# Optimization experiments

Hardware: AMD Instinct MI355X
Metric: run time of the kernel (lower is better)

The kernel has to match this reference:

```python
import jax, jax.numpy as jnp
import numpy as np

FM = 64      # feature_maps
QM = 64      # query_maps
ROUNDS = 16  # test_rounds (training=False path)
NV = 50000   # n_vars
NC = 210000  # n_clauses
NE = 630000  # literal-clause edges (3-SAT)
NG = 32      # batched graphs
EPS = 1e-6


def _leaky(x):
    return jax.nn.leaky_relu(x, negative_slope=0.2)


def _mlp2(x, W0, b0, W1, b1):
    return _leaky(x @ W0 + b0) @ W1 + b1


def _mlp3(x, W0, b0, W1, b1, W2, b2):
    return _leaky(_leaky(x @ W0 + b0) @ W1 + b1) @ W2 + b2


def _pair_norm(x, seg, n_seg):
    # PairNorm with per-graph mean subtraction and per-graph variance scaling
    cnt = jax.ops.segment_sum(jnp.ones((x.shape[0], 1), x.dtype), seg, num_segments=n_seg)
    mean = jax.ops.segment_sum(x, seg, num_segments=n_seg) / cnt
    xc = x - mean[seg]
    var = jax.ops.segment_sum(xc * xc, seg, num_segments=n_seg) / cnt
    return xc * jax.lax.rsqrt(var + EPS)[seg]


def _glorot(k, shape):
    return (jax.random.normal(k, shape) * np.sqrt(2.0 / (shape[0] + shape[1]))).astype(jnp.float32)


def setup_inputs() -> dict:
    key = jax.random.key(0)
    ks = jax.random.split(key, 16)
    lit_idx = jax.random.randint(ks[0], (NE,), 0, 2 * NV)
    clause_idx = jnp.repeat(jnp.arange(NC), NE // NC)  # 3 literals per clause
    var_gid = jnp.sort(jax.random.randint(ks[1], (NV,), 0, NG))
    clause_gid = jnp.sort(jax.random.randint(ks[2], (NC,), 0, NG))
    noise = jax.random.normal(ks[3], (ROUNDS, NV, 4), dtype=jnp.float32)
    inp = dict(lit_idx=lit_idx, clause_idx=clause_idx, var_gid=var_gid,
               clause_gid=clause_gid, noise=noise)
    # variables_query: MLP(2, QM, QM), input FM+4
    inp['qW0'] = _glorot(ks[4], (FM + 4, QM)); inp['qb0'] = jnp.zeros((QM,), jnp.float32)
    inp['qW1'] = _glorot(ks[5], (QM, QM));     inp['qb1'] = jnp.zeros((QM,), jnp.float32)
    # clause_mlp: MLP(2, 2*FM, FM+QM), input FM+QM
    inp['cW0'] = _glorot(ks[6], (FM + QM, 2 * FM));   inp['cb0'] = jnp.zeros((2 * FM,), jnp.float32)
    inp['cW1'] = _glorot(ks[7], (2 * FM, FM + QM));   inp['cb1'] = jnp.zeros((FM + QM,), jnp.float32)
    # update_gate: MLP(3, 2*FM, FM), input QM+FM+QM+QM
    inp['uW0'] = _glorot(ks[8], (FM + 3 * QM, 2 * FM)); inp['ub0'] = jnp.zeros((2 * FM,), jnp.float32)
    inp['uW1'] = _glorot(ks[9], (2 * FM, 2 * FM));      inp['ub1'] = jnp.zeros((2 * FM,), jnp.float32)
    inp['uW2'] = _glorot(ks[10], (2 * FM, FM));         inp['ub2'] = jnp.zeros((FM,), jnp.float32)
    # clauses_output: MLP(2, FM, 1)
    inp['oW0'] = _glorot(ks[11], (FM, FM)); inp['ob0'] = jnp.zeros((FM,), jnp.float32)
    inp['oW1'] = _glorot(ks[12], (FM, 1));  inp['ob1'] = jnp.zeros((1,), jnp.float32)
    return inp


def reference(lit_idx, clause_idx, var_gid, clause_gid, noise,
              qW0, qb0, qW1, qb1, cW0, cb0, cW1, cb1,
              uW0, ub0, uW1, ub1, uW2, ub2, oW0, ob0, oW1, ob1):
    # literal degrees: sparse row-sums of adj_matrix
    lit_degree = jax.ops.segment_sum(jnp.ones((NE,), jnp.float32), lit_idx,
                                     num_segments=2 * NV)[:, None]  # [2V,1]
    degree_weight = jax.lax.rsqrt(jnp.maximum(lit_degree, 1.0))
    var_degree_weight = 4.0 * jax.lax.rsqrt(jnp.maximum(lit_degree[:NV] + lit_degree[NV:], 1.0))

    def clause_loss_fn(query):
        # unsat_cnf_clauses_loss: clause value = exp(-sum softplus(lit))
        lits = jax.nn.softplus(jnp.concatenate([query, -query], axis=0))  # [2V,QM]
        cv = jax.ops.segment_sum(lits[lit_idx], clause_idx, num_segments=NC)
        return jnp.exp(-cv)  # [C,QM]

    def step_loss_fn(query):
        cl = clause_loss_fn(query)
        return jnp.sum(cl), cl

    def body(carry, noise_t):
        variables, clauses = carry
        v1 = jnp.concatenate([variables, noise_t], axis=-1)          # [V, FM+4]
        query = _mlp2(v1, qW0, qb0, qW1, qb1)                        # [V, QM]
        (_, clauses_loss), vgrad = jax.value_and_grad(step_loss_fn, has_aux=True)(query)
        vgrad = vgrad * var_degree_weight
        clauses_loss = clauses_loss * 4.0
        clause_unit = jnp.concatenate([clauses, clauses_loss], axis=-1)  # [C, FM+QM]
        clause_data = _mlp2(clause_unit, cW0, cb0, cW1, cb1)             # [C, FM+QM]
        variables_loss_all = clause_data[:, :QM]
        new_clause = _pair_norm(clause_data[:, QM:], clause_gid, NG) * 0.25
        clauses = new_clause + 0.1 * clauses
        # variables_loss = adj_matrix @ variables_loss_all  (gather per edge, scatter to literals)
        variables_loss = jax.ops.segment_sum(variables_loss_all[clause_idx], lit_idx,
                                             num_segments=2 * NV) * degree_weight
        unit = jnp.concatenate([vgrad, variables, variables_loss[:NV], variables_loss[NV:]], axis=-1)
        new_vars = _pair_norm(_mlp3(unit, uW0, ub0, uW1, ub1, uW2, ub2), var_gid, NG) * 0.25
        variables = new_vars + 0.1 * variables
        logits = _mlp2(clauses, oW0, ob0, oW1, ob1)  # [C,1]
        variables = jax.lax.stop_gradient(variables) * 0.2 + variables * 0.8
        clauses = jax.lax.stop_gradient(clauses) * 0.2 + clauses * 0.8
        return (variables, clauses), logits

    init = (jnp.ones((NV, FM), jnp.float32), jnp.ones((NC, FM), jnp.float32))
    _, step_logits = jax.lax.scan(body, init, noise)
    last_logits = step_logits[-1]  # inference path: last round's logits [C,1]
    return (jnp.squeeze(jax.nn.sigmoid(last_logits), axis=-1),
            jnp.squeeze(jax.nn.softplus(last_logits), axis=-1))
```

## Files before the change

### kernel.cpp

```cpp
#include <hip/hip_runtime.h>
#include <math.h>

typedef unsigned short u16;
typedef unsigned int u32;
typedef _Float16 f16;
typedef f16 f16x8 __attribute__((ext_vector_type(8)));
typedef f16 f16x4 __attribute__((ext_vector_type(4)));
typedef float f32x4 __attribute__((ext_vector_type(4)));

constexpr int kNV = 50000;
constexpr int kNC = 210000;
constexpr int kNE = 630000;
constexpr int kNG = 32;
constexpr int kRounds = 16;
constexpr float kEps = 1e-6f;

constexpr int kCmlpB = (kNC + 63)/64;
constexpr int kVmlpB = (kNV + 63)/64;
constexpr int kUpdCB = kNC*64/1024;

__device__ __forceinline__ float bf2f(u16 v){ return __uint_as_float(((u32)v)<<16); }
__device__ __forceinline__ u16 f2bf(float f){
  u32 x = __float_as_uint(f);
  x += 0x7FFFu + ((x>>16)&1u);
  return (u16)(x>>16);
}
__device__ __forceinline__ u16 f2h(float v){
  union { f16 h; u16 u; } cv; cv.h = (f16)v; return cv.u;
}
__device__ __forceinline__ float h2f(u16 v){
  union { u16 u; f16 h; } cv; cv.u = v; return (float)cv.h;
}
__device__ __forceinline__ float leaky(float x){ return x>0.f ? x : 0.2f*x; }
__device__ __forceinline__ float softplusf(float x){
  return fmaxf(x,0.f) + __logf(1.f + __expf(-fabsf(x)));
}

struct Buf { void* p; int f32; };
__device__ __forceinline__ float ldb(Buf b, size_t i){
  return b.f32 ? ((const float*)b.p)[i] : bf2f(((const u16*)b.p)[i]);
}
__device__ __forceinline__ void stb(Buf b, size_t i, float v){
  if (b.f32) ((float*)b.p)[i] = v; else ((u16*)b.p)[i] = f2bf(v);
}
__device__ __forceinline__ float4 ldb4(Buf b, size_t i){
  if (b.f32) return *(const float4*)((const float*)b.p + i);
  u32 a = *(const u32*)((const u16*)b.p + i);
  u32 c = *(const u32*)((const u16*)b.p + i + 2);
  float4 r; r.x=bf2f((u16)a); r.y=bf2f((u16)(a>>16)); r.z=bf2f((u16)c); r.w=bf2f((u16)(c>>16));
  return r;
}
__device__ __forceinline__ void stb4(Buf b, size_t i, float4 v){
  if (b.f32){ *(float4*)((float*)b.p + i) = v; return; }
  u32 a = (u32)f2bf(v.x) | ((u32)f2bf(v.y)<<16);
  u32 c = (u32)f2bf(v.z) | ((u32)f2bf(v.w)<<16);
  *(u32*)((u16*)b.p + i) = a; *(u32*)((u16*)b.p + i + 2) = c;
}

constexpr int WP_C0 = 0;
constexpr int WP_C1 = 16384;
constexpr int WP_U0 = 32768;
constexpr int WP_U1 = 65536;
constexpr int WP_U2 = 81920;
constexpr int WP_Q0 = 90112;
constexpr int WP_Q1 = 96256;
constexpr int WP_TOT= 100352;

#define XS_STR 136

__global__ __launch_bounds__(256) void k_init(Buf vars, Buf cls, int* cnt, int* cur,
                                              double* stats, int* vst, int* ven,
                                              int* cst, int* cen){
  int i = blockIdx.x*256 + threadIdx.x;
  if (i < kNV*64) stb(vars, i, 1.f);
  stb(cls, i, 1.f);
  if (i < 2*kNV){ cnt[i]=0; cur[i]=0; }
  if (i < 16384) stats[i]=0.0;
  if (i < kNG){ vst[i]=0; ven[i]=0; cst[i]=0; cen[i]=0; }
}

__global__ __launch_bounds__(256) void k_wprep(
  const float* __restrict__ cW0, const float* __restrict__ cW1,
  const float* __restrict__ uW0, const float* __restrict__ uW1,
  const float* __restrict__ uW2,
  const float* __restrict__ qW0, const float* __restrict__ qW1,
  u16* __restrict__ wp){
  int i = blockIdx.x*256 + threadIdx.x;
  if (i < 16384){ int n=i>>7, k=i&127; wp[i] = f2h(cW0[k*128+n]); }
  else if (i < 32768){ int j=i-16384; int n=j>>7, k=j&127; wp[i] = f2h(cW1[k*128+n]); }
  else if (i < 65536){ int j=i-32768; int n=j>>8, k=j&255; wp[i] = f2h(uW0[k*128+n]); }
  else if (i < 81920){ int j=i-65536; int n=j>>7, k=j&127; wp[i] = f2h(uW1[k*128+n]); }
  else if (i < 90112){ int j=i-81920; int n=j>>7, k=j&127; wp[i] = f2h(uW2[k*64+n]); }
  else if (i < 96256){ int j=i-90112; int n=j/96, k=j%96; wp[i] = (k<68)? f2h(qW0[k*64+n]) : (u16)0; }
  else if (i < WP_TOT){ int j=i-96256; int n=j>>6, k=j&63; wp[i] = f2h(qW1[k*64+n]); }
}

__global__ __launch_bounds__(256) void k_hist(const int* __restrict__ lit,
                                              const int* __restrict__ vgid,
// ... 43 lines not shown
  if (i < 2*kNV){
    rs[i] += bsum[blockIdx.x];
    int c = cnt[i]; if (c<1) c=1;
    dw[i] = rsqrtf((float)c);
  }
  if (i < kNV){
    int c = cnt[i] + cnt[i+kNV]; if (c<1) c=1;
    vdw[i] = 4.f*rsqrtf((float)c);
  }
}

__global__ __launch_bounds__(256) void k_fill(const int* __restrict__ lit,
                                              const int* __restrict__ cidx,
                                              const int* __restrict__ rs, int* cur, int* csr){
  int e = blockIdx.x*256 + threadIdx.x;
  if (e < kNE){
    int l = lit[e];
    int p = atomicAdd(&cur[l], 1);
    csr[rs[l]+p] = cidx[e];
  }
}

__global__ __launch_bounds__(256) void k_query(
  Buf vars, const float* __restrict__ noise_r,
  const u16* __restrict__ Q0T, const u16* __restrict__ Q1T,
  f16* __restrict__ SP,
  Buf nvb, const int* __restrict__ vgid,
  const int* __restrict__ vst, const int* __restrict__ ven,
  const double* __restrict__ vSo, const double* __restrict__ vQo,
  double* __restrict__ zstats, int round)
{
  __shared__ __align__(16) u16 xs[64*104];
  __shared__ float ms[2*64], is[2*64];
  const int tid = threadIdx.x;
  if (blockIdx.x < 32) zstats[blockIdx.x*256 + tid] = 0.0;
  const int lane = tid & 63, wv = tid >> 6;
  const int qd = lane >> 4, mr = lane & 15;
  const int base = blockIdx.x * 64;
  int g0 = 0, gend0 = 0x7fffffff;
  if (round > 0){
    int rl = base+63; if (rl >= kNV) rl = kNV-1;
    g0 = vgid[base];
    int ng = vgid[rl]-g0+1; if (ng > 2) ng = 2;
    gend0 = ven[g0];
    for (int e=tid; e<ng*64; e+=256){
      int g = g0 + (e>>6), f = e&63;
      int c = ven[g]-vst[g];
      float m=0.f, iv=0.f;
      if (c > 0){
        double S=vSo[g*64+f], Q=vQo[g*64+f];
        double md=S/c, var=Q/c-md*md; if (var<0.0) var=0.0;
        m=(float)md; iv=rsqrtf((float)var + kEps);
      }
      ms[e]=m; is[e]=iv;
    }
  }
  for (int v=0; v<4; ++v){
    int idx = v*256 + tid;
    if (idx < 896){
      int row = idx/14, cw = idx%14;
      *(u32*)&xs[row*104 + 68 + cw*2] = 0;
    }
  }
  __syncthreads();
  for (int v4=0; v4<4; ++v4){
    int idx = (v4*256 + tid)*4;
    int row = idx>>6, col = idx&63;
    int gr = base + row;
    bool own = (gr < kNV); if (!own) gr = kNV-1;
    float4 x;
    if (round > 0){
      float4 nv = ldb4(nvb,  (size_t)gr*64 + col);
      float4 vo = ldb4(vars, (size_t)gr*64 + col);
      int gl = (gr >= gend0) ? 1 : 0;
      const float* mp = &ms[gl*64+col]; const float* ip = &is[gl*64+col];
      x.x = (nv.x-mp[0])*ip[0]*0.25f + 0.1f*vo.x;
      x.y = (nv.y-mp[1])*ip[1]*0.25f + 0.1f*vo.y;
      x.z = (nv.z-mp[2])*ip[2]*0.25f + 0.1f*vo.z;
      x.w = (nv.w-mp[3])*ip[3]*0.25f + 0.1f*vo.w;
      if (own) stb4(vars, (size_t)gr*64 + col, x);
    } else {
      x = ldb4(vars, (size_t)gr*64 + col);
    }
    uint2 pk; pk.x = (u32)f2h(x.x)|((u32)f2h(x.y)<<16); pk.y = (u32)f2h(x.z)|((u32)f2h(x.w)<<16);
    *(uint2*)&xs[row*104 + col] = pk;
  }
  {
    int row = tid>>2, c = tid&3;
    int gr = base + row; if (gr >= kNV) gr = kNV-1;
    xs[row*104 + 64 + c] = f2h(noise_r[(size_t)gr*4 + c]);
  }
  __syncthreads();
  f32x4 acc[4] = {};
  #pragma unroll 1
  for (int ks=0; ks<3; ++ks){
    f16x8 av = *(const f16x8*)&xs[(wv*16+mr)*104 + ks*32 + qd*8];
    #pragma unroll
    for (int n=0;n<4;++n){
      f16x8 bv = *(const f16x8*)&Q0T[(n*16+mr)*96 + ks*32 + qd*8];
      acc[n] = __builtin_amdgcn_mfma_f32_16x16x32_f16(av, bv, acc[n], 0,0,0);
    }
  }
  __syncthreads();
  #pragma unroll
  for (int n=0;n<4;++n) for (int r=0;r<4;++r)
    xs[(wv*16 + qd*4 + r)*104 + n*16 + mr] = f2h(leaky(acc[n][r]));
  #pragma unroll
  for (int n=0;n<4;++n) for (int r=0;r<4;++r) acc[n][r] = 0.f;
// ... 1 lines not shown
  #pragma unroll 1
  for (int ks=0; ks<2; ++ks){
    f16x8 av = *(const f16x8*)&xs[(wv*16+mr)*104 + ks*32 + qd*8];
    #pragma unroll
    for (int n=0;n<4;++n){
      f16x8 bv = *(const f16x8*)&Q1T[(n*16+mr)*64 + ks*32 + qd*8];
      acc[n] = __builtin_amdgcn_mfma_f32_16x16x32_f16(av, bv, acc[n], 0,0,0);
    }
  }
  #pragma unroll
  for (int n=0;n<4;++n) for (int r=0;r<4;++r){
    int row = base + wv*16 + qd*4 + r;
    if (row < kNV){
      float v = acc[n][r];
      float sneg = 1.f/(1.f + __expf(v));
      float spos = 1.f - sneg;
      SP[(size_t)row*64 + n*16 + mr]       = (f16)sneg;
      SP[(size_t)(kNV+row)*64 + n*16 + mr] = (f16)spos;
    }
  }
}

__global__ __launch_bounds__(256) void k_clause_mlp(
  const f16* __restrict__ SP, const int* __restrict__ lit, Buf cls,
  const u16* __restrict__ W0T, const u16* __restrict__ W1T,
  u16* __restrict__ clcda, Buf cdb,
  const int* __restrict__ cgid,
  double* __restrict__ gsum, double* __restrict__ gsq,
  const int* __restrict__ cst, const int* __restrict__ cen,
  const double* __restrict__ cSo, const double* __restrict__ cQo,
  int round)
{
  __shared__ __align__(16) u16 xs[64*XS_STR];
  __shared__ __align__(16) u16 clbuf[64*64];
  __shared__ float cms[2*64], cis[2*64];
  const int tid = threadIdx.x;
  const int lane = tid & 63, wv = tid >> 6;
  const int qd = lane >> 4, mr = lane & 15;
  const int base = blockIdx.x * 64;
  const int mt0 = (wv>>1)*2, ntA = (wv&1)*4;
  const int g0 = cgid[base];
  int gend0 = 0x7fffffff;
  if (round > 0){
    int rl = base+63; if (rl >= kNC) rl = kNC-1;
    int ng = cgid[rl]-g0+1; if (ng > 2) ng = 2;
    gend0 = cen[g0];
    for (int e=tid; e<ng*64; e+=256){
      int g = g0 + (e>>6), f = e&63;
      int c = cen[g]-cst[g];
      float m=0.f, iv=0.f;
      if (c > 0){
        double S=cSo[g*64+f], Q=cQo[g*64+f];
        double md=S/c, var=Q/c-md*md; if (var<0.0) var=0.0;
        m=(float)md; iv=rsqrtf((float)var + kEps);
      }
      cms[e]=m; cis[e]=iv;
    }
  }
  __syncthreads();
  for (int v4=0; v4<4; ++v4){
    int idx = (v4*256 + tid)*4;
    int row = idx>>6, col = idx&63;
    int gr = base + row;
    bool own = (gr < kNC); if (!own) gr = kNC-1;
    float4 x;
    if (round > 0){
      float4 cd = ldb4(cdb, (size_t)gr*64 + col);
      float4 co = ldb4(cls, (size_t)gr*64 + col);
      int gl = (gr >= gend0) ? 1 : 0;
      const float* mp = &cms[gl*64+col]; const float* ip = &cis[gl*64+col];
      x.x = (cd.x-mp[0])*ip[0]*0.25f + 0.1f*co.x;
      x.y = (cd.y-mp[1])*ip[1]*0.25f + 0.1f*co.y;
      x.z = (cd.z-mp[2])*ip[2]*0.25f + 0.1f*co.z;
      x.w = (cd.w-mp[3])*ip[3]*0.25f + 0.1f*co.w;
      if (own) stb4(cls, (size_t)gr*64 + col, x);
    } else {
      x = ldb4(cls, (size_t)gr*64 + col);
    }
    uint2 pk;
    pk.x = (u32)f2h(x.x)|((u32)f2h(x.y)<<16);
    pk.y = (u32)f2h(x.z)|((u32)f2h(x.w)<<16);
    *(uint2*)&xs[row*XS_STR + col] = pk;
  }
  {
    int row = tid>>2, cq = tid&3;
    int gr = base + row; if (gr >= kNC) gr = kNC-1;
    int l0 = lit[3*gr], l1 = lit[3*gr+1], l2 = lit[3*gr+2];
    const f16* p0 = &SP[(size_t)l0*64 + cq*16];
    const f16* p1 = &SP[(size_t)l1*64 + cq*16];
    const f16* p2 = &SP[(size_t)l2*64 + cq*16];
    f16x8 aa = *(const f16x8*)p0, ab = *(const f16x8*)(p0+8);
    f16x8 ba = *(const f16x8*)p1, bb = *(const f16x8*)(p1+8);
    f16x8 ca = *(const f16x8*)p2, cb2= *(const f16x8*)(p2+8);
    f16x8 cl0 = aa*ba*ca, cl1 = ab*bb*cb2;
    *(f16x8*)&clbuf[row*64 + cq*16]     = cl0;
    *(f16x8*)&clbuf[row*64 + cq*16 + 8] = cl1;
    f16x8 x0 = cl0+cl0; x0 = x0+x0;
    f16x8 x1 = cl1+cl1; x1 = x1+x1;
    *(f16x8*)&xs[row*XS_STR + 64 + cq*16]     = x0;
    *(f16x8*)&xs[row*XS_STR + 64 + cq*16 + 8] = x1;
  }
  __syncthreads();
  f32x4 acc[2][4] = {};
  #pragma unroll 1
  for (int ks=0; ks<4; ++ks){
    f16x8 av[2], bv[4];
    #pragma unroll
    for (int m=0;m<2;++m)
      av[m] = *(const f16x8*)&xs[((mt0+m)*16+mr)*XS_STR + ks*32 + qd*8];
    #pragma unroll
    for (int n=0;n<4;++n)
      bv[n] = *(const f16x8*)&W0T[((ntA+n)*16+mr)*128 + ks*32 + qd*8];
    #pragma unroll
    for (int m=0;m<2;++m)
      #pragma unroll
      for (int n=0;n<4;++n)
        acc[m][n] = __builtin_amdgcn_mfma_f32_16x16x32_f16(av[m], bv[n], acc[m][n], 0,0,0);
  }
  __syncthreads();
// ... 2 lines not shown
    xs[((mt0+m)*16 + qd*4 + r)*XS_STR + (ntA+n)*16 + mr] = f2h(leaky(acc[m][n][r]));
  #pragma unroll
  for (int m=0;m<2;++m) for (int n=0;n<4;++n) for (int r=0;r<4;++r) acc[m][n][r] = 0.f;
  __syncthreads();
  #pragma unroll 1
  for (int ks=0; ks<4; ++ks){
    f16x8 av[2], bv[4];
    #pragma unroll
    for (int m=0;m<2;++m)
      av[m] = *(const f16x8*)&xs[((mt0+m)*16+mr)*XS_STR + ks*32 + qd*8];
    #pragma unroll
    for (int n=0;n<4;++n)
      bv[n] = *(const f16x8*)&W1T[((ntA+n)*16+mr)*128 + ks*32 + qd*8];
    #pragma unroll
    for (int m=0;m<2;++m)
      #pragma unroll
      for (int n=0;n<4;++n)
        acc[m][n] = __builtin_amdgcn_mfma_f32_16x16x32_f16(av[m], bv[n], acc[m][n], 0,0,0);
  }
  #pragma unroll
  for (int m=0;m<2;++m) for (int r=0;r<4;++r){
    int row = base + (mt0+m)*16 + qd*4 + r;
    if (row >= kNC) continue;
    int lrow = (mt0+m)*16 + qd*4 + r;
    #pragma unroll
    for (int n=0;n<4;++n){
      float v = acc[m][n][r];
      int cc = (ntA+n)*16 + mr;
      if (cc < 64){
        u32 pk = (u32)clbuf[lrow*64 + cc] | ((u32)f2bf(v)<<16);
        *(u32*)&clcda[(size_t)row*128 + 2*cc] = pk;
      } else {
        stb(cdb, (size_t)row*64+cc-64, v);
      }
    }
  }
  __syncthreads();
  float* lsum = (float*)xs;
  float* lsq  = lsum + 256;
  for (int i=tid; i<512; i+=256) lsum[i] = 0.f;
  __syncthreads();
  if (ntA == 4){
    float s[4], sq[4];
    int gc = -1;
    #pragma unroll
    for (int n=0;n<4;++n){ s[n]=0.f; sq[n]=0.f; }
    auto flush = [&](){
      if (gc < 4){
        #pragma unroll
        for (int n=0;n<4;++n){
          if (s[n] != 0.f)  atomicAdd(&lsum[gc*64 + n*16 + mr], s[n]);
          if (sq[n] != 0.f) atomicAdd(&lsq [gc*64 + n*16 + mr], sq[n]);
        }
      } else {
        int g = g0 + gc;
        if (g < kNG){
          #pragma unroll
          for (int n=0;n<4;++n){
            atomicAdd(&gsum[g*64 + n*16 + mr], (double)s[n]);
            atomicAdd(&gsq [g*64 + n*16 + mr], (double)sq[n]);
          }
        }
      }
    };
// ... 10 lines not shown
            #pragma unroll
            for (int n=0;n<4;++n){ s[n]=0.f; sq[n]=0.f; }
          }
          #pragma unroll
          for (int n=0;n<4;++n){ float v = acc[m][n][r]; s[n]+=v; sq[n]+=v*v; }
        }
      }
    }
    if (gc >= 0) flush();
  }
  __syncthreads();
  {
    int g = g0 + (tid>>6);
    if (g < kNG){
      float v = lsum[tid], w = lsq[tid];
      if (v != 0.f) atomicAdd(&gsum[g*64 + (tid&63)], (double)v);
      if (w != 0.f) atomicAdd(&gsq [g*64 + (tid&63)], (double)w);
    }
  }
}

__global__ __launch_bounds__(256) void k_litsum2(
  const int* __restrict__ rs, const int* __restrict__ cnt, const int* __restrict__ csr,
  const u16* __restrict__ clcda, const float* __restrict__ dw,
  Buf SL, Buf VL)
{
  const int w = threadIdx.x>>6, f = threadIdx.x&63;
  const int l = blockIdx.x*4 + w;
  const int beg = rs[l], n = cnt[l];
  float s1 = 0.f, s2 = 0.f;
  int j = 0;
  for (; j+4 <= n; j += 4){
    int c0 = csr[beg+j], c1 = csr[beg+j+1], c2 = csr[beg+j+2], c3 = csr[beg+j+3];
    u32 a0 = *(const u32*)&clcda[(size_t)c0*128 + 2*f];
    u32 a1 = *(const u32*)&clcda[(size_t)c1*128 + 2*f];
    u32 a2 = *(const u32*)&clcda[(size_t)c2*128 + 2*f];
    u32 a3 = *(const u32*)&clcda[(size_t)c3*128 + 2*f];
    s1 += h2f((u16)a0) + h2f((u16)a1) + h2f((u16)a2) + h2f((u16)a3);
    s2 += bf2f((u16)(a0>>16)) + bf2f((u16)(a1>>16)) + bf2f((u16)(a2>>16)) + bf2f((u16)(a3>>16));
  }
  for (; j < n; ++j){
    int c = csr[beg+j];
    u32 a = *(const u32*)&clcda[(size_t)c*128 + 2*f];
    s1 += h2f((u16)a);
    s2 += bf2f((u16)(a>>16));
  }
  stb(SL, (size_t)l*64+f, s1);
  stb(VL, (size_t)l*64+f, s2 * dw[l]);
}

__global__ __launch_bounds__(256) void k_var_mlp(
  const f16* __restrict__ SP, Buf SL, Buf VL, Buf vars, const float* __restrict__ vdw,
  const u16* __restrict__ U0T, const u16* __restrict__ U1T, const u16* __restrict__ U2T,
  Buf nvb, const int* __restrict__ vgid,
  double* __restrict__ gsum, double* __restrict__ gsq)
{
  __shared__ __align__(16) u16 xs[64*XS_STR];
  const int tid = threadIdx.x;
  const int lane = tid & 63, wv = tid >> 6;
  const int qd = lane >> 4, mr = lane & 15;
  const int base = blockIdx.x * 64;
  const int mt0 = (wv>>1)*2, ntA = (wv&1)*4;
  f32x4 acc[2][4] = {};
  #pragma unroll 1
  for (int half=0; half<2; ++half){
    if (half) __syncthreads();
    if (half == 0){
      for (int v4=0; v4<4; ++v4){
        int idx = (v4*256 + tid)*4;
        int row = idx>>6, col = idx&63;
        int gr = base + row; if (gr >= kNV) gr = kNV-1;
        float vw = vdw[gr];
        f16x4 spv = *(const f16x4*)&SP[(size_t)(kNV+gr)*64 + col];
        float4 sl = ldb4(SL, (size_t)gr*64 + col);
        float4 sn = ldb4(SL, (size_t)(kNV+gr)*64 + col);
        float o[4];
        float pa[4] = {sl.x,sl.y,sl.z,sl.w};
        float na[4] = {sn.x,sn.y,sn.z,sn.w};
        #pragma unroll
        for (int t=0;t<4;++t){
          float sp = (float)spv[t];
          o[t] = vw*((1.f-sp)*na[t] - sp*pa[t]);
        }
        uint2 pk;
        pk.x = (u32)f2h(o[0])|((u32)f2h(o[1])<<16);
        pk.y = (u32)f2h(o[2])|((u32)f2h(o[3])<<16);
        *(uint2*)&xs[row*XS_STR + col] = pk;
      }
      for (int v4=0; v4<4; ++v4){
        int idx = (v4*256 + tid)*4;
        int row = idx>>6, col = idx&63;
        int gr = base + row; if (gr >= kNV) gr = kNV-1;
        float4 x = ldb4(vars, (size_t)gr*64 + col);
        uint2 pk;
        pk.x = (u32)f2h(x.x)|((u32)f2h(x.y)<<16);
        pk.y = (u32)f2h(x.z)|((u32)f2h(x.w)<<16);
        *(uint2*)&xs[row*XS_STR + 64 + col] = pk;
      }
    } else {
      #pragma unroll
      for (int t=0; t<2; ++t){
        for (int v4=0; v4<4; ++v4){
          int idx = (v4*256 + tid)*4;
          int row = idx>>6, col = idx&63;
          int gr = base + row; if (gr >= kNV) gr = kNV-1;
          float4 x = ldb4(VL, (size_t)(t ? kNV+gr : gr)*64 + col);
          uint2 pk;
          pk.x = (u32)f2h(x.x)|((u32)f2h(x.y)<<16);
          pk.y = (u32)f2h(x.z)|((u32)f2h(x.w)<<16);
          *(uint2*)&xs[row*XS_STR + t*64 + col] = pk;
        }
      }
    }
    __syncthreads();
    #pragma unroll 1
    for (int ks=0; ks<4; ++ks){
      f16x8 av[2], bv[4];
      #pragma unroll
      for (int m=0;m<2;++m)
        av[m] = *(const f16x8*)&xs[((mt0+m)*16+mr)*XS_STR + ks*32 + qd*8];
      #pragma unroll
      for (int n=0;n<4;++n)
        bv[n] = *(const f16x8*)&U0T[((ntA+n)*16+mr)*256 + half*128 + ks*32 + qd*8];
      #pragma unroll
      for (int m=0;m<2;++m)
        #pragma unroll
        for (int n=0;n<4;++n)
          acc[m][n] = __builtin_amdgcn_mfma_f32_16x16x32_f16(av[m], bv[n], acc[m][n], 0,0,0);
    }
  }
  __syncthreads();
  #pragma unroll
  for (int m=0;m<2;++m) for (int n=0;n<4;++n) for (int r=0;r<4;++r)
// ... 24 lines not shown
  for (int m=0;m<2;++m) for (int n=0;n<4;++n) for (int r=0;r<4;++r) acc[m][n][r] = 0.f;
  __syncthreads();
  const int nt3 = (wv&1)*2;
  #pragma unroll 1
  for (int ks=0; ks<4; ++ks){
    f16x8 av[2], bv[2];
    #pragma unroll
    for (int m=0;m<2;++m)
      av[m] = *(const f16x8*)&xs[((mt0+m)*16+mr)*XS_STR + ks*32 + qd*8];
    #pragma unroll
    for (int n=0;n<2;++n)
      bv[n] = *(const f16x8*)&U2T[((nt3+n)*16+mr)*128 + ks*32 + qd*8];
    #pragma unroll
    for (int m=0;m<2;++m)
      #pragma unroll
      for (int n=0;n<2;++n)
        acc[m][n] = __builtin_amdgcn_mfma_f32_16x16x32_f16(av[m], bv[n], acc[m][n], 0,0,0);
  }
  #pragma unroll
  for (int m=0;m<2;++m) for (int r=0;r<4;++r){
    int row = base + (mt0+m)*16 + qd*4 + r;
    if (row >= kNV) continue;
    #pragma unroll
    for (int n=0;n<2;++n) stb(nvb, (size_t)row*64 + (nt3+n)*16 + mr, acc[m][n][r]);
  }
  __syncthreads();
  float* lsum = (float*)xs;
  float* lsq  = lsum + 256;
  for (int i=tid; i<512; i+=256) lsum[i] = 0.f;
  __syncthreads();
  const int g0 = vgid[base];
  {
    float s[2], sq[2];
    int gc = -1;
    s[0]=s[1]=0.f; sq[0]=sq[1]=0.f;
    auto flush = [&](){
      if (gc < 4){
        #pragma unroll
        for (int n=0;n<2;++n){
          if (s[n] != 0.f)  atomicAdd(&lsum[gc*64 + (nt3+n)*16 + mr], s[n]);
          if (sq[n] != 0.f) atomicAdd(&lsq [gc*64 + (nt3+n)*16 + mr], sq[n]);
        }
      } else {
        int g = g0 + gc;
        if (g < kNG){
          #pragma unroll
          for (int n=0;n<2;++n){
            atomicAdd(&gsum[g*64 + (nt3+n)*16 + mr], (double)s[n]);
            atomicAdd(&gsq [g*64 + (nt3+n)*16 + mr], (double)sq[n]);
          }
        }
      }
    };
// ... 7 lines not shown
          if (gl != gc){
            if (gc >= 0) flush();
            gc = gl;
            s[0]=s[1]=0.f; sq[0]=sq[1]=0.f;
          }
          #pragma unroll
          for (int n=0;n<2;++n){ float v = acc[m][n][r]; s[n]+=v; sq[n]+=v*v; }
        }
      }
    }
    if (gc >= 0) flush();
  }
  __syncthreads();
  {
    int g = g0 + (tid>>6);
    if (g < kNG){
      float v = lsum[tid], w = lsq[tid];
      if (v != 0.f) atomicAdd(&gsum[g*64 + (tid&63)], (double)v);
      if (w != 0.f) atomicAdd(&gsq [g*64 + (tid&63)], (double)w);
    }
  }
}

__global__ __launch_bounds__(256) void k_upd(
  Buf x, const int* __restrict__ gid,
  const int* __restrict__ gst, const int* __restrict__ gen,
  const double* __restrict__ gsum, const double* __restrict__ gsq,
  Buf state, int nelem)
{
  __shared__ float ms[6*64], is[6*64];
  const int tid = threadIdx.x;
  const int base = blockIdx.x*1024;
  const int nrows = nelem>>6;
  int r0 = base>>6;
  int rl = (base+1023)>>6; if (rl >= nrows) rl = nrows-1;
  int g0 = gid[r0];
  int ng = gid[rl]-g0+1; if (ng > 6) ng = 6;
  for (int e=tid; e<ng*64; e+=256){
    int g = g0 + (e>>6), f = e&63;
    int c = gen[g]-gst[g];
    float m=0.f, iv=0.f;
    if (c > 0){
      double S=gsum[g*64+f], Q=gsq[g*64+f];
      double md=S/c, var=Q/c-md*md; if (var<0.0) var=0.0;
      m=(float)md; iv=rsqrtf((float)var + kEps);
    }
    ms[e]=m; is[e]=iv;
  }
  __syncthreads();
  int i4 = base + tid*4;
  if (i4 >= nelem) return;
  int row = i4>>6, f = i4&63;
  int gr = gid[row]-g0; if (gr > 5) gr = 5;
  float4 v = ldb4(x, i4);
  float4 s = ldb4(state, i4);
  const float* mp = &ms[gr*64+f]; const float* ip = &is[gr*64+f];
  s.x = (v.x-mp[0])*ip[0]*0.25f + 0.1f*s.x;
  s.y = (v.y-mp[1])*ip[1]*0.25f + 0.1f*s.y;
  s.z = (v.z-mp[2])*ip[2]*0.25f + 0.1f*s.z;
  s.w = (v.w-mp[3])*ip[3]*0.25f + 0.1f*s.w;
  stb4(state, i4, s);
}

__global__ __launch_bounds__(256) void k_logits(
  Buf cls,
  const float* __restrict__ oW0, const float* __restrict__ oW1,
  float* __restrict__ out)
{
  __shared__ float w0s[64*64];
  __shared__ float w1s[64];
  __shared__ __align__(16) float xb[64][64];
  const int tid = threadIdx.x;
  for (int i=tid;i<64*64;i+=256) w0s[i]=oW0[i];
  if (tid<64) w1s[tid]=oW1[tid];
  const int wv=tid>>6, f=tid&63;
  const int base = blockIdx.x*64;
  for (int v4=0; v4<4; ++v4){
    int idx = (v4*256 + tid)*4;
    int row = idx>>6, col = idx&63;
    int gr = base + row; if (gr >= kNC) gr = kNC-1;
    *(float4*)&xb[row][col] = ldb4(cls, (size_t)gr*64 + col);
  }
  __syncthreads();
  const int r0 = wv*16;
  float a[16];
  #pragma unroll
  for (int r=0;r<16;++r) a[r] = 0.f;
  for (int k=0;k<64;k+=4){
    float w4[4];
    #pragma unroll
    for (int i=0;i<4;++i) w4[i] = w0s[(k+i)*64+f];
    #pragma unroll
    for (int r=0;r<16;++r){
      float4 xv = *(const float4*)&xb[r0+r][k];
      a[r] = fmaf(xv.x, w4[0], a[r]);
      a[r] = fmaf(xv.y, w4[1], a[r]);
      a[r] = fmaf(xv.z, w4[2], a[r]);
      a[r] = fmaf(xv.w, w4[3], a[r]);
    }
  }
  float w1 = w1s[f];
  #pragma unroll 1
  for (int r=0;r<16;++r){
    float t = leaky(a[r]) * w1;
// ... 11 lines not shown

extern "C" void kernel_launch(void* const* d_in, const int* in_sizes, int n_in,
                              void* d_out, int out_size, void* d_ws, size_t ws_size,
                              hipStream_t stream)
{
  const int* lit   = (const int*)d_in[0];
  const int* cidx  = (const int*)d_in[1];
  const int* vgid  = (const int*)d_in[2];
  const int* cgid  = (const int*)d_in[3];
  const float* noise = (const float*)d_in[4];
  const float* qW0=(const float*)d_in[5];
  const float* qW1=(const float*)d_in[7];
  const float* cW0=(const float*)d_in[9];
  const float* cW1=(const float*)d_in[11];
  const float* uW0=(const float*)d_in[13];
  const float* uW1=(const float*)d_in[15];
  const float* uW2=(const float*)d_in[17];
  const float* oW0=(const float*)d_in[19];
  const float* oW1=(const float*)d_in[21];
  float* out = (float*)d_out;

  const size_t NVF = (size_t)kNV*64;
  const size_t NCF = (size_t)kNC*64;
  const size_t cnts[9] = {NCF, 2*NVF, 2*NCF, 0, 2*NVF, 2*NVF, NVF, NCF, NVF};
  auto al = [](size_t x){ return (x + 255) & ~(size_t)255; };
  const size_t smallsN = (size_t)2*kNV + kNV;
  const size_t dblN    = (size_t)16384;
  const size_t intN    = (size_t)3*2*kNV + kNE + 128 + 4*kNG;
  const size_t tail = al(smallsN*4) + al(dblN*8) + al(intN*4) + al((size_t)WP_TOT*2);
  bool f32[9] = {false,false,false,false,false,false,false,false,false};
  size_t need = tail;
  for (int i=0;i<9;++i) need += al(cnts[i]*2);
  const int prio[4] = {0, 6, 7, 8};
  for (int pi=0; pi<4; ++pi){
    int t = prio[pi];
    size_t extra = al(cnts[t]*4) - al(cnts[t]*2);
    if (need + extra <= ws_size){ f32[t] = true; need += extra; }
  }
  size_t off = 0, boff[9];
  for (int i=0;i<9;++i){ boff[i] = off; off = al(off + cnts[i]*(f32[i]?4:2)); }
  float*  Fp = (float*)((char*)d_ws + off);  off = al(off + smallsN*4);
  double* Dp = (double*)((char*)d_ws + off); off = al(off + dblN*8);
  int*    Ip = (int*)((char*)d_ws + off);    off = al(off + intN*4);
  u16*    wp = (u16*)((char*)d_ws + off);

  Buf CLS { (char*)d_ws + boff[0], f32[0] };
  f16* SPp = (f16*)((char*)d_ws + boff[1]);
  u16* CLCDA = (u16*)((char*)d_ws + boff[2]);
  Buf SL  { (char*)d_ws + boff[4], f32[4] };
  Buf VL  { (char*)d_ws + boff[5], f32[5] };
  Buf VARS{ (char*)d_ws + boff[6], f32[6] };
  Buf CDB { (char*)d_ws + boff[7], f32[7] };
  Buf NVB { (char*)d_ws + boff[8], f32[8] };

  float* dw = Fp;                    float* vdw = Fp + 2*kNV;
  double* cS[2] = { Dp,            Dp + 8192 };
  double* cQ[2] = { Dp + 2048,     Dp + 10240 };
  double* vS[2] = { Dp + 4096,     Dp + 12288 };
  double* vQ[2] = { Dp + 6144,     Dp + 14336 };
  int* cnt = Ip;            int* rs  = cnt + 2*kNV;  int* cur = rs + 2*kNV;
  int* csr = cur + 2*kNV;   int* bsum= csr + kNE;    int* vst = bsum + 128;
  int* ven = vst + kNG;     int* cst = ven + kNG;    int* cen = cst + kNG;

  k_init<<<kNC*64/256, 256, 0, stream>>>(VARS, CLS, cnt, cur, Dp, vst, ven, cst, cen);
  k_wprep<<<(WP_TOT+255)/256, 256, 0, stream>>>(cW0, cW1, uW0, uW1, uW2, qW0, qW1, wp);
  k_hist<<<(kNE+255)/256, 256, 0, stream>>>(lit, vgid, cgid, cnt, vst, ven, cst, cen);
  k_scan1<<<98, 1024, 0, stream>>>(cnt, rs, bsum);
  k_scan2<<<1, 32, 0, stream>>>(bsum, 98);
  k_scan3<<<98, 1024, 0, stream>>>(cnt, rs, bsum, dw, vdw);
  k_fill<<<(kNE+255)/256, 256, 0, stream>>>(lit, cidx, rs, cur, csr);

  for (int r=0; r<kRounds; ++r){
    const int p = r & 1, o = 1 - p;
    const float* noise_r = noise + (size_t)r*kNV*4;
    k_query<<<kVmlpB, 256, 0, stream>>>(VARS, noise_r, wp+WP_Q0, wp+WP_Q1, SPp,
                                        NVB, vgid, vst, ven, vS[o], vQ[o],
                                        Dp + (size_t)p*8192, r);
    k_clause_mlp<<<kCmlpB, 256, 0, stream>>>(SPp, lit, CLS, wp+WP_C0, wp+WP_C1,
                                             CLCDA, CDB, cgid, cS[p], cQ[p],
                                             cst, cen, cS[o], cQ[o], r);
    if (r < kRounds-1){
      k_litsum2<<<2*kNV/4, 256, 0, stream>>>(rs, cnt, csr, CLCDA, dw, SL, VL);
      k_var_mlp<<<kVmlpB, 256, 0, stream>>>(SPp, SL, VL, VARS, vdw,
                                            wp+WP_U0, wp+WP_U1, wp+WP_U2, NVB, vgid,
                                            vS[p], vQ[p]);
    }
  }
  k_upd<<<kUpdCB, 256, 0, stream>>>(CDB, cgid, cst, cen,
                                    cS[(kRounds-1)&1], cQ[(kRounds-1)&1], CLS, kNC*64);
  k_logits<<<kCmlpB, 256, 0, stream>>>(CLS, oW0, oW1, out);
}
```

Baseline: 3.644 ms.

## Store all state buffers in fp16 and fuse final clause update into logits

Replaces the runtime-selected bf16/fp32 state buffers with fixed fp16 storage, so the per-element format branches and bf16 conversions go away and the raw fp16 can be copied straight into LDS. The clause MLP now writes the clause-product half of CLCDA directly instead of staging it in shared memory, keeps a separate LDS stats area so two barriers can be dropped, and skips the CLCDA writes in the last round. The final k_upd kernel is folded into k_logits. Storing state in fp16 lowers memory traffic but may cost range and precision compared with the fp32 buffers used when workspace allowed.

```diff
diff --git a/kernel.cpp b/kernel.cpp
--- a/kernel.cpp
+++ b/kernel.cpp
@@ -17,44 +17,22 @@
 
 constexpr int kCmlpB = (kNC + 63)/64;
 constexpr int kVmlpB = (kNV + 63)/64;
-constexpr int kUpdCB = kNC*64/1024;
-
-__device__ __forceinline__ float bf2f(u16 v){ return __uint_as_float(((u32)v)<<16); }
-__device__ __forceinline__ u16 f2bf(float f){
-  u32 x = __float_as_uint(f);
-  x += 0x7FFFu + ((x>>16)&1u);
-  return (u16)(x>>16);
-}
+
 __device__ __forceinline__ u16 f2h(float v){
   union { f16 h; u16 u; } cv; cv.h = (f16)v; return cv.u;
-}
-__device__ __forceinline__ float h2f(u16 v){
-  union { u16 u; f16 h; } cv; cv.u = v; return (float)cv.h;
 }
 __device__ __forceinline__ float leaky(float x){ return x>0.f ? x : 0.2f*x; }
 __device__ __forceinline__ float softplusf(float x){
   return fmaxf(x,0.f) + __logf(1.f + __expf(-fabsf(x)));
 }
-
-struct Buf { void* p; int f32; };
-__device__ __forceinline__ float ldb(Buf b, size_t i){
-  return b.f32 ? ((const float*)b.p)[i] : bf2f(((const u16*)b.p)[i]);
-}
-__device__ __forceinline__ void stb(Buf b, size_t i, float v){
-  if (b.f32) ((float*)b.p)[i] = v; else ((u16*)b.p)[i] = f2bf(v);
-}
-__device__ __forceinline__ float4 ldb4(Buf b, size_t i){
-  if (b.f32) return *(const float4*)((const float*)b.p + i);
-  u32 a = *(const u32*)((const u16*)b.p + i);
-  u32 c = *(const u32*)((const u16*)b.p + i + 2);
-  float4 r; r.x=bf2f((u16)a); r.y=bf2f((u16)(a>>16)); r.z=bf2f((u16)c); r.w=bf2f((u16)(c>>16));
+__device__ __forceinline__ float4 ld4h(const f16* p, size_t i){
+  f16x4 v = *(const f16x4*)(p + i);
+  float4 r; r.x=(float)v[0]; r.y=(float)v[1]; r.z=(float)v[2]; r.w=(float)v[3];
   return r;
 }
-__device__ __forceinline__ void stb4(Buf b, size_t i, float4 v){
-  if (b.f32){ *(float4*)((float*)b.p + i) = v; return; }
-  u32 a = (u32)f2bf(v.x) | ((u32)f2bf(v.y)<<16);
-  u32 c = (u32)f2bf(v.z) | ((u32)f2bf(v.w)<<16);
-  *(u32*)((u16*)b.p + i) = a; *(u32*)((u16*)b.p + i + 2) = c;
+__device__ __forceinline__ void st4h(f16* p, size_t i, float4 v){
+  f16x4 o; o[0]=(f16)v.x; o[1]=(f16)v.y; o[2]=(f16)v.z; o[3]=(f16)v.w;
+  *(f16x4*)(p + i) = o;
 }
 
 constexpr int WP_C0 = 0;
@@ -68,12 +46,12 @@
 
 #define XS_STR 136
 
-__global__ __launch_bounds__(256) void k_init(Buf vars, Buf cls, int* cnt, int* cur,
+__global__ __launch_bounds__(256) void k_init(f16* vars, f16* cls, int* cnt, int* cur,
                                               double* stats, int* vst, int* ven,
                                               int* cst, int* cen){
   int i = blockIdx.x*256 + threadIdx.x;
-  if (i < kNV*64) stb(vars, i, 1.f);
-  stb(cls, i, 1.f);
+  if (i < kNV*64) vars[i] = (f16)1.f;
+  cls[i] = (f16)1.f;
   if (i < 2*kNV){ cnt[i]=0; cur[i]=0; }
   if (i < 16384) stats[i]=0.0;
   if (i < kNG){ vst[i]=0; ven[i]=0; cst[i]=0; cen[i]=0; }
@@ -163,10 +141,10 @@
 }
 
 __global__ __launch_bounds__(256) void k_query(
-  Buf vars, const float* __restrict__ noise_r,
+  f16* __restrict__ vars, const float* __restrict__ noise_r,
   const u16* __restrict__ Q0T, const u16* __restrict__ Q1T,
   f16* __restrict__ SP,
-  Buf nvb, const int* __restrict__ vgid,
+  const f16* __restrict__ nvb, const int* __restrict__ vgid,
   const int* __restrict__ vst, const int* __restrict__ ven,
   const double* __restrict__ vSo, const double* __restrict__ vQo,
   double* __restrict__ zstats, int round)
@@ -178,10 +156,10 @@
   const int lane = tid & 63, wv = tid >> 6;
   const int qd = lane >> 4, mr = lane & 15;
   const int base = blockIdx.x * 64;
-  int g0 = 0, gend0 = 0x7fffffff;
+  int gend0 = 0x7fffffff;
   if (round > 0){
     int rl = base+63; if (rl >= kNV) rl = kNV-1;
-    g0 = vgid[base];
+    int g0 = vgid[base];
     int ng = vgid[rl]-g0+1; if (ng > 2) ng = 2;
     gend0 = ven[g0];
     for (int e=tid; e<ng*64; e+=256){
@@ -209,22 +187,22 @@
     int row = idx>>6, col = idx&63;
     int gr = base + row;
     bool own = (gr < kNV); if (!own) gr = kNV-1;
-    float4 x;
     if (round > 0){
-      float4 nv = ldb4(nvb,  (size_t)gr*64 + col);
-      float4 vo = ldb4(vars, (size_t)gr*64 + col);
+      float4 nv = ld4h(nvb,  (size_t)gr*64 + col);
+      float4 vo = ld4h(vars, (size_t)gr*64 + col);
       int gl = (gr >= gend0) ? 1 : 0;
       const float* mp = &ms[gl*64+col]; const float* ip = &is[gl*64+col];
+      float4 x;
       x.x = (nv.x-mp[0])*ip[0]*0.25f + 0.1f*vo.x;
       x.y = (nv.y-mp[1])*ip[1]*0.25f + 0.1f*vo.y;
       x.z = (nv.z-mp[2])*ip[2]*0.25f + 0.1f*vo.z;
       x.w = (nv.w-mp[3])*ip[3]*0.25f + 0.1f*vo.w;
-      if (own) stb4(vars, (size_t)gr*64 + col, x);
+      if (own) st4h(vars, (size_t)gr*64 + col, x);
+      uint2 pk; pk.x = (u32)f2h(x.x)|((u32)f2h(x.y)<<16); pk.y = (u32)f2h(x.z)|((u32)f2h(x.w)<<16);
+      *(uint2*)&xs[row*104 + col] = pk;
     } else {
-      x = ldb4(vars, (size_t)gr*64 + col);
-    }
-    uint2 pk; pk.x = (u32)f2h(x.x)|((u32)f2h(x.y)<<16); pk.y = (u32)f2h(x.z)|((u32)f2h(x.w)<<16);
-    *(uint2*)&xs[row*104 + col] = pk;
+      *(uint2*)&xs[row*104 + col] = *(const uint2*)&vars[(size_t)gr*64 + col];
+    }
   }
   {
     int row = tid>>2, c = tid&3;
@@ -272,18 +250,18 @@
 }
 
 __global__ __launch_bounds__(256) void k_clause_mlp(
-  const f16* __restrict__ SP, const int* __restrict__ lit, Buf cls,
+  const f16* __restrict__ SP, const int* __restrict__ lit, f16* __restrict__ cls,
   const u16* __restrict__ W0T, const u16* __restrict__ W1T,
-  u16* __restrict__ clcda, Buf cdb,
+  f16* __restrict__ clcda, f16* __restrict__ cdb,
   const int* __restrict__ cgid,
   double* __restrict__ gsum, double* __restrict__ gsq,
   const int* __restrict__ cst, const int* __restrict__ cen,
   const double* __restrict__ cSo, const double* __restrict__ cQo,
-  int round)
+  int round, int last)
 {
   __shared__ __align__(16) u16 xs[64*XS_STR];
-  __shared__ __align__(16) u16 clbuf[64*64];
   __shared__ float cms[2*64], cis[2*64];
+  __shared__ float lstat[512];
   const int tid = threadIdx.x;
   const int lane = tid & 63, wv = tid >> 6;
   const int qd = lane >> 4, mr = lane & 15;
@@ -307,34 +285,36 @@
       cms[e]=m; cis[e]=iv;
     }
   }
+  lstat[tid] = 0.f; lstat[tid+256] = 0.f;
   __syncthreads();
   for (int v4=0; v4<4; ++v4){
     int idx = (v4*256 + tid)*4;
     int row = idx>>6, col = idx&63;
     int gr = base + row;
     bool own = (gr < kNC); if (!own) gr = kNC-1;
-    float4 x;
     if (round > 0){
-      float4 cd = ldb4(cdb, (size_t)gr*64 + col);
-      float4 co = ldb4(cls, (size_t)gr*64 + col);
+      float4 cd = ld4h(cdb, (size_t)gr*64 + col);
+      float4 co = ld4h(cls, (size_t)gr*64 + col);
       int gl = (gr >= gend0) ? 1 : 0;
       const float* mp = &cms[gl*64+col]; const float* ip = &cis[gl*64+col];
+      float4 x;
       x.x = (cd.x-mp[0])*ip[0]*0.25f + 0.1f*co.x;
       x.y = (cd.y-mp[1])*ip[1]*0.25f + 0.1f*co.y;
       x.z = (cd.z-mp[2])*ip[2]*0.25f + 0.1f*co.z;
       x.w = (cd.w-mp[3])*ip[3]*0.25f + 0.1f*co.w;
-      if (own) stb4(cls, (size_t)gr*64 + col, x);
+      if (own) st4h(cls, (size_t)gr*64 + col, x);
+      uint2 pk;
+      pk.x = (u32)f2h(x.x)|((u32)f2h(x.y)<<16);
+      pk.y = (u32)f2h(x.z)|((u32)f2h(x.w)<<16);
+      *(uint2*)&xs[row*XS_STR + col] = pk;
     } else {
-      x = ldb4(cls, (size_t)gr*64 + col);
-    }
-    uint2 pk;
-    pk.x = (u32)f2h(x.x)|((u32)f2h(x.y)<<16);
-    pk.y = (u32)f2h(x.z)|((u32)f2h(x.w)<<16);
-    *(uint2*)&xs[row*XS_STR + col] = pk;
+      *(uint2*)&xs[row*XS_STR + col] = *(const uint2*)&cls[(size_t)gr*64 + col];
+    }
   }
   {
     int row = tid>>2, cq = tid&3;
-    int gr = base + row; if (gr >= kNC) gr = kNC-1;
+    int gr = base + row;
+    bool own = (gr < kNC); if (!own) gr = kNC-1;
     int l0 = lit[3*gr], l1 = lit[3*gr+1], l2 = lit[3*gr+2];
     const f16* p0 = &SP[(size_t)l0*64 + cq*16];
     const f16* p1 = &SP[(size_t)l1*64 + cq*16];
@@ -343,8 +323,10 @@
     f16x8 ba = *(const f16x8*)p1, bb = *(const f16x8*)(p1+8);
     f16x8 ca = *(const f16x8*)p2, cb2= *(const f16x8*)(p2+8);
     f16x8 cl0 = aa*ba*ca, cl1 = ab*bb*cb2;
-    *(f16x8*)&clbuf[row*64 + cq*16]     = cl0;
-    *(f16x8*)&clbuf[row*64 + cq*16 + 8] = cl1;
+    if (!last && own){
+      *(f16x8*)&clcda[(size_t)gr*128 + cq*16]     = cl0;
+      *(f16x8*)&clcda[(size_t)gr*128 + cq*16 + 8] = cl1;
+    }
     f16x8 x0 = cl0+cl0; x0 = x0+x0;
     f16x8 x1 = cl1+cl1; x1 = x1+x1;
     *(f16x8*)&xs[row*XS_STR + 64 + cq*16]     = x0;
@@ -393,24 +375,20 @@
   for (int m=0;m<2;++m) for (int r=0;r<4;++r){
     int row = base + (mt0+m)*16 + qd*4 + r;
     if (row >= kNC) continue;
-    int lrow = (mt0+m)*16 + qd*4 + r;
-    #pragma unroll
-    for (int n=0;n<4;++n){
-      float v = acc[m][n][r];
-      int cc = (ntA+n)*16 + mr;
-      if (cc < 64){
-        u32 pk = (u32)clbuf[lrow*64 + cc] | ((u32)f2bf(v)<<16);
-        *(u32*)&clcda[(size_t)row*128 + 2*cc] = pk;
-      } else {
-        stb(cdb, (size_t)row*64+cc-64, v);
-      }
-    }
-  }
-  __syncthreads();
-  float* lsum = (float*)xs;
-  float* lsq  = lsum + 256;
-  for (int i=tid; i<512; i+=256) lsum[i] = 0.f;
-  __syncthreads();
+    if (ntA == 0){
+      if (!last){
+        #pragma unroll
+        for (int n=0;n<4;++n)
+          clcda[(size_t)row*128 + 64 + n*16 + mr] = (f16)acc[m][n][r];
+      }
+    } else {
+      #pragma unroll
+      for (int n=0;n<4;++n)
+        cdb[(size_t)row*64 + n*16 + mr] = (f16)acc[m][n][r];
+    }
+  }
+  float* lsum = lstat;
+  float* lsq  = lstat + 256;
   if (ntA == 4){
     float s[4], sq[4];
     int gc = -1;
@@ -467,8 +445,8 @@
 
 __global__ __launch_bounds__(256) void k_litsum2(
   const int* __restrict__ rs, const int* __restrict__ cnt, const int* __restrict__ csr,
-  const u16* __restrict__ clcda, const float* __restrict__ dw,
-  Buf SL, Buf VL)
+  const f16* __restrict__ clcda, const float* __restrict__ dw,
+  f16* __restrict__ SL, f16* __restrict__ VL)
 {
   const int w = threadIdx.x>>6, f = threadIdx.x&63;
   const int l = blockIdx.x*4 + w;
@@ -477,35 +455,35 @@
   int j = 0;
   for (; j+4 <= n; j += 4){
     int c0 = csr[beg+j], c1 = csr[beg+j+1], c2 = csr[beg+j+2], c3 = csr[beg+j+3];
-    u32 a0 = *(const u32*)&clcda[(size_t)c0*128 + 2*f];
-    u32 a1 = *(const u32*)&clcda[(size_t)c1*128 + 2*f];
-    u32 a2 = *(const u32*)&clcda[(size_t)c2*128 + 2*f];
-    u32 a3 = *(const u32*)&clcda[(size_t)c3*128 + 2*f];
-    s1 += h2f((u16)a0) + h2f((u16)a1) + h2f((u16)a2) + h2f((u16)a3);
-    s2 += bf2f((u16)(a0>>16)) + bf2f((u16)(a1>>16)) + bf2f((u16)(a2>>16)) + bf2f((u16)(a3>>16));
+    s1 += (float)clcda[(size_t)c0*128 + f] + (float)clcda[(size_t)c1*128 + f]
+        + (float)clcda[(size_t)c2*128 + f] + (float)clcda[(size_t)c3*128 + f];
+    s2 += (float)clcda[(size_t)c0*128 + 64 + f] + (float)clcda[(size_t)c1*128 + 64 + f]
+        + (float)clcda[(size_t)c2*128 + 64 + f] + (float)clcda[(size_t)c3*128 + 64 + f];
   }
   for (; j < n; ++j){
     int c = csr[beg+j];
-    u32 a = *(const u32*)&clcda[(size_t)c*128 + 2*f];
-    s1 += h2f((u16)a);
-    s2 += bf2f((u16)(a>>16));
-  }
-  stb(SL, (size_t)l*64+f, s1);
-  stb(VL, (size_t)l*64+f, s2 * dw[l]);
+    s1 += (float)clcda[(size_t)c*128 + f];
+    s2 += (float)clcda[(size_t)c*128 + 64 + f];
+  }
+  SL[(size_t)l*64+f] = (f16)s1;
+  VL[(size_t)l*64+f] = (f16)(s2 * dw[l]);
 }
 
 __global__ __launch_bounds__(256) void k_var_mlp(
-  const f16* __restrict__ SP, Buf SL, Buf VL, Buf vars, const float* __restrict__ vdw,
+  const f16* __restrict__ SP, const f16* __restrict__ SL, const f16* __restrict__ VL,
+  const f16* __restrict__ vars, const float* __restrict__ vdw,
   const u16* __restrict__ U0T, const u16* __restrict__ U1T, const u16* __restrict__ U2T,
-  Buf nvb, const int* __restrict__ vgid,
+  f16* __restrict__ nvb, const int* __restrict__ vgid,
   double* __restrict__ gsum, double* __restrict__ gsq)
 {
   __shared__ __align__(16) u16 xs[64*XS_STR];
+  __shared__ float lstat[512];
   const int tid = threadIdx.x;
   const int lane = tid & 63, wv = tid >> 6;
   const int qd = lane >> 4, mr = lane & 15;
   const int base = blockIdx.x * 64;
   const int mt0 = (wv>>1)*2, ntA = (wv&1)*4;
+  lstat[tid] = 0.f; lstat[tid+256] = 0.f;
   f32x4 acc[2][4] = {};
   #pragma unroll 1
   for (int half=0; half<2; ++half){
@@ -517,8 +495,8 @@
         int gr = base + row; if (gr >= kNV) gr = kNV-1;
         float vw = vdw[gr];
         f16x4 spv = *(const f16x4*)&SP[(size_t)(kNV+gr)*64 + col];
-        float4 sl = ldb4(SL, (size_t)gr*64 + col);
-        float4 sn = ldb4(SL, (size_t)(kNV+gr)*64 + col);
+        float4 sl = ld4h(SL, (size_t)gr*64 + col);
+        float4 sn = ld4h(SL, (size_t)(kNV+gr)*64 + col);
         float o[4];
         float pa[4] = {sl.x,sl.y,sl.z,sl.w};
         float na[4] = {sn.x,sn.y,sn.z,sn.w};
@@ -536,11 +514,7 @@
         int idx = (v4*256 + tid)*4;
         int row = idx>>6, col = idx&63;
         int gr = base + row; if (gr >= kNV) gr = kNV-1;
-        float4 x = ldb4(vars, (size_t)gr*64 + col);
-        uint2 pk;
-        pk.x = (u32)f2h(x.x)|((u32)f2h(x.y)<<16);
-        pk.y = (u32)f2h(x.z)|((u32)f2h(x.w)<<16);
-        *(uint2*)&xs[row*XS_STR + 64 + col] = pk;
+        *(uint2*)&xs[row*XS_STR + 64 + col] = *(const uint2*)&vars[(size_t)gr*64 + col];
       }
     } else {
       #pragma unroll
@@ -549,11 +523,8 @@
           int idx = (v4*256 + tid)*4;
           int row = idx>>6, col = idx&63;
           int gr = base + row; if (gr >= kNV) gr = kNV-1;
-          float4 x = ldb4(VL, (size_t)(t ? kNV+gr : gr)*64 + col);
-          uint2 pk;
-          pk.x = (u32)f2h(x.x)|((u32)f2h(x.y)<<16);
-          pk.y = (u32)f2h(x.z)|((u32)f2h(x.w)<<16);
-          *(uint2*)&xs[row*XS_STR + t*64 + col] = pk;
+          *(uint2*)&xs[row*XS_STR + t*64 + col] =
+            *(const uint2*)&VL[(size_t)(t ? kNV+gr : gr)*64 + col];
         }
       }
     }
@@ -624,13 +595,10 @@
     int row = base + (mt0+m)*16 + qd*4 + r;
     if (row >= kNV) continue;
     #pragma unroll
-    for (int n=0;n<2;++n) stb(nvb, (size_t)row*64 + (nt3+n)*16 + mr, acc[m][n][r]);
-  }
-  __syncthreads();
-  float* lsum = (float*)xs;
-  float* lsq  = lsum + 256;
-  for (int i=tid; i<512; i+=256) lsum[i] = 0.f;
-  __syncthreads();
+    for (int n=0;n<2;++n) nvb[(size_t)row*64 + (nt3+n)*16 + mr] = (f16)acc[m][n][r];
+  }
+  float* lsum = lstat;
+  float* lsq  = lstat + 256;
   const int g0 = vgid[base];
   {
     float s[2], sq[2];
@@ -684,64 +652,55 @@
   }
 }
 
-__global__ __launch_bounds__(256) void k_upd(
-  Buf x, const int* __restrict__ gid,
-  const int* __restrict__ gst, const int* __restrict__ gen,
+__global__ __launch_bounds__(256) void k_logits(
+  const f16* __restrict__ cdb, const f16* __restrict__ cls,
+  const int* __restrict__ cgid,
+  const int* __restrict__ cst, const int* __restrict__ cen,
   const double* __restrict__ gsum, const double* __restrict__ gsq,
-  Buf state, int nelem)
-{
-  __shared__ float ms[6*64], is[6*64];
-  const int tid = threadIdx.x;
-  const int base = blockIdx.x*1024;
-  const int nrows = nelem>>6;
-  int r0 = base>>6;
-  int rl = (base+1023)>>6; if (rl >= nrows) rl = nrows-1;
-  int g0 = gid[r0];
-  int ng = gid[rl]-g0+1; if (ng > 6) ng = 6;
-  for (int e=tid; e<ng*64; e+=256){
-    int g = g0 + (e>>6), f = e&63;
-    int c = gen[g]-gst[g];
-    float m=0.f, iv=0.f;
-    if (c > 0){
-      double S=gsum[g*64+f], Q=gsq[g*64+f];
-      double md=S/c, var=Q/c-md*md; if (var<0.0) var=0.0;
-      m=(float)md; iv=rsqrtf((float)var + kEps);
-    }
-    ms[e]=m; is[e]=iv;
-  }
-  __syncthreads();
-  int i4 = base + tid*4;
-  if (i4 >= nelem) return;
-  int row = i4>>6, f = i4&63;
-  int gr = gid[row]-g0; if (gr > 5) gr = 5;
-  float4 v = ldb4(x, i4);
-  float4 s = ldb4(state, i4);
-  const float* mp = &ms[gr*64+f]; const float* ip = &is[gr*64+f];
-  s.x = (v.x-mp[0])*ip[0]*0.25f + 0.1f*s.x;
-  s.y = (v.y-mp[1])*ip[1]*0.25f + 0.1f*s.y;
-  s.z = (v.z-mp[2])*ip[2]*0.25f + 0.1f*s.z;
-  s.w = (v.w-mp[3])*ip[3]*0.25f + 0.1f*s.w;
-  stb4(state, i4, s);
-}
-
-__global__ __launch_bounds__(256) void k_logits(
-  Buf cls,
   const float* __restrict__ oW0, const float* __restrict__ oW1,
   float* __restrict__ out)
 {
   __shared__ float w0s[64*64];
   __shared__ float w1s[64];
   __shared__ __align__(16) float xb[64][64];
+  __shared__ float cms[2*64], cis[2*64];
   const int tid = threadIdx.x;
+  const int base = blockIdx.x*64;
+  const int g0 = cgid[base];
+  {
+    int rl = base+63; if (rl >= kNC) rl = kNC-1;
+    int ng = cgid[rl]-g0+1; if (ng > 2) ng = 2;
+    for (int e=tid; e<ng*64; e+=256){
+      int g = g0 + (e>>6), f = e&63;
+      int c = cen[g]-cst[g];
+      float m=0.f, iv=0.f;
+      if (c > 0){
+        double S=gsum[g*64+f], Q=gsq[g*64+f];
+        double md=S/c, var=Q/c-md*md; if (var<0.0) var=0.0;
+        m=(float)md; iv=rsqrtf((float)var + kEps);
+      }
+      cms[e]=m; cis[e]=iv;
+    }
+  }
+  const int gend0 = cen[g0];
   for (int i=tid;i<64*64;i+=256) w0s[i]=oW0[i];
   if (tid<64) w1s[tid]=oW1[tid];
+  __syncthreads();
   const int wv=tid>>6, f=tid&63;
-  const int base = blockIdx.x*64;
   for (int v4=0; v4<4; ++v4){
     int idx = (v4*256 + tid)*4;
     int row = idx>>6, col = idx&63;
     int gr = base + row; if (gr >= kNC) gr = kNC-1;
-    *(float4*)&xb[row][col] = ldb4(cls, (size_t)gr*64 + col);
+    float4 cd = ld4h(cdb, (size_t)gr*64 + col);
+    float4 co = ld4h(cls, (size_t)gr*64 + col);
+    int gl = (gr >= gend0) ? 1 : 0;
+    const float* mp = &cms[gl*64+col]; const float* ip = &cis[gl*64+col];
+    float4 x;
+    x.x = (cd.x-mp[0])*ip[0]*0.25f + 0.1f*co.x;
+    x.y = (cd.y-mp[1])*ip[1]*0.25f + 0.1f*co.y;
+    x.z = (cd.z-mp[2])*ip[2]*0.25f + 0.1f*co.z;
+    x.w = (cd.w-mp[3])*ip[3]*0.25f + 0.1f*co.w;
+    *(float4*)&xb[row][col] = x;
   }
   __syncthreads();
   const int r0 = wv*16;
@@ -799,36 +758,24 @@
 
   const size_t NVF = (size_t)kNV*64;
   const size_t NCF = (size_t)kNC*64;
-  const size_t cnts[9] = {NCF, 2*NVF, 2*NCF, 0, 2*NVF, 2*NVF, NVF, NCF, NVF};
   auto al = [](size_t x){ return (x + 255) & ~(size_t)255; };
+  size_t off = 0;
+  auto alloc_h = [&](size_t n)->f16*{ f16* p = (f16*)((char*)d_ws + off); off = al(off + n*2); return p; };
+  f16* CLS   = alloc_h(NCF);
+  f16* SPp   = alloc_h(2*NVF);
+  f16* CLCDA = alloc_h(2*NCF);
+  f16* SL    = alloc_h(2*NVF);
+  f16* VL    = alloc_h(2*NVF);
+  f16* VARS  = alloc_h(NVF);
+  f16* CDB   = alloc_h(NCF);
+  f16* NVB   = alloc_h(NVF);
   const size_t smallsN = (size_t)2*kNV + kNV;
   const size_t dblN    = (size_t)16384;
   const size_t intN    = (size_t)3*2*kNV + kNE + 128 + 4*kNG;
-  const size_t tail = al(smallsN*4) + al(dblN*8) + al(intN*4) + al((size_t)WP_TOT*2);
-  bool f32[9] = {false,false,false,false,false,false,false,false,false};
-  size_t need = tail;
-  for (int i=0;i<9;++i) need += al(cnts[i]*2);
-  const int prio[4] = {0, 6, 7, 8};
-  for (int pi=0; pi<4; ++pi){
-    int t = prio[pi];
-    size_t extra = al(cnts[t]*4) - al(cnts[t]*2);
-    if (need + extra <= ws_size){ f32[t] = true; need += extra; }
-  }
-  size_t off = 0, boff[9];
-  for (int i=0;i<9;++i){ boff[i] = off; off = al(off + cnts[i]*(f32[i]?4:2)); }
   float*  Fp = (float*)((char*)d_ws + off);  off = al(off + smallsN*4);
   double* Dp = (double*)((char*)d_ws + off); off = al(off + dblN*8);
   int*    Ip = (int*)((char*)d_ws + off);    off = al(off + intN*4);
   u16*    wp = (u16*)((char*)d_ws + off);
-
-  Buf CLS { (char*)d_ws + boff[0], f32[0] };
-  f16* SPp = (f16*)((char*)d_ws + boff[1]);
-  u16* CLCDA = (u16*)((char*)d_ws + boff[2]);
-  Buf SL  { (char*)d_ws + boff[4], f32[4] };
-  Buf VL  { (char*)d_ws + boff[5], f32[5] };
-  Buf VARS{ (char*)d_ws + boff[6], f32[6] };
-  Buf CDB { (char*)d_ws + boff[7], f32[7] };
-  Buf NVB { (char*)d_ws + boff[8], f32[8] };
 
   float* dw = Fp;                    float* vdw = Fp + 2*kNV;
   double* cS[2] = { Dp,            Dp + 8192 };
@@ -855,7 +802,8 @@
                                         Dp + (size_t)p*8192, r);
     k_clause_mlp<<<kCmlpB, 256, 0, stream>>>(SPp, lit, CLS, wp+WP_C0, wp+WP_C1,
                                              CLCDA, CDB, cgid, cS[p], cQ[p],
-                                             cst, cen, cS[o], cQ[o], r);
+                                             cst, cen, cS[o], cQ[o], r,
+                                             (r==kRounds-1) ? 1 : 0);
     if (r < kRounds-1){
       k_litsum2<<<2*kNV/4, 256, 0, stream>>>(rs, cnt, csr, CLCDA, dw, SL, VL);
       k_var_mlp<<<kVmlpB, 256, 0, stream>>>(SPp, SL, VL, VARS, vdw,
@@ -863,7 +811,7 @@
                                             vS[p], vQ[p]);
     }
   }
-  k_upd<<<kUpdCB, 256, 0, stream>>>(CDB, cgid, cst, cen,
-                                    cS[(kRounds-1)&1], cQ[(kRounds-1)&1], CLS, kNC*64);
-  k_logits<<<kCmlpB, 256, 0, stream>>>(CLS, oW0, oW1, out);
-}
+  k_logits<<<kCmlpB, 256, 0, stream>>>(CDB, CLS, cgid, cst, cen,
+                                       cS[(kRounds-1)&1], cQ[(kRounds-1)&1],
+                                       oW0, oW1, out);
+}
```

After: 3.226 ms. 11.5% less time.
